# Optimization experiments

Measured on AMD Instinct MI355X. Metric: run time of the kernel, lower is better.

Reference implementation:

```python
import jax, jax.numpy as jnp
import numpy as np

TEMPERATURE = 0.07
NEG = -1e9  # stand-in for -inf on the diagonal; exp(NEG) == 0


def setup_inputs() -> dict:
    key = jax.random.key(0)
    k1, k2, k3 = jax.random.split(key, 3)
    B, D = 4096, 1024
    return {
        "anchor_features": jax.random.normal(k1, (B, D), dtype=jnp.float32),
        "positive_features": jax.random.normal(k2, (B, D), dtype=jnp.float32),
        "labels": jax.random.randint(k3, (B,), 0, 2),
    }


def reference(anchor_features, positive_features, labels):
    B = anchor_features.shape[0]
    # L2-normalize (normalize=True)
    a = anchor_features / jnp.linalg.norm(anchor_features, axis=1, keepdims=True)
    p = positive_features / jnp.linalg.norm(positive_features, axis=1, keepdims=True)
    feats = jnp.concatenate([a, p], axis=0)                      # [2B, D]
    sim = jnp.matmul(feats, feats.T) / TEMPERATURE               # [2B, 2B]
    diag = jnp.eye(2 * B, dtype=bool)
    sim = jnp.where(diag, NEG, sim)                              # mask self-similarity
    # logsumexp over all non-self entries per row (diag contributes exp(NEG)=0)
    lse = jax.nn.logsumexp(sim, axis=1)                          # [2B]
    # positive pair similarity: sim[i, i+B] == sim[i+B, i] == <a_i, p_i>/t
    cross = jnp.sum(a * p, axis=1) / TEMPERATURE                 # [B]
    pos_sim = jnp.concatenate([cross, cross])                    # [2B]
    lab = jnp.concatenate([labels, labels]).astype(sim.dtype)    # [2B], 0/1
    per_row = (-pos_sim + lse) * lab
    num_pos = jnp.sum(lab)
    return jnp.where(num_pos > 0, jnp.sum(per_row) / num_pos, jnp.float32(0.0))
```

## Files before the change

kernel.cpp:

```cpp
#include <hip/hip_runtime.h>
#include <hip/hip_bf16.h>

#define TEMP_INV (1.0f / 0.07f)
#define LOG2E 1.4426950408889634f
#define LN2 0.6931471805599453f
#define CFIX 21.0f

typedef __attribute__((ext_vector_type(4))) float f32x4;

__device__ __forceinline__ void gload16(const unsigned char* g,
                                        unsigned char* l) {
  __builtin_amdgcn_global_load_lds(
      (const __attribute__((address_space(1))) void*)g,
      (__attribute__((address_space(3))) void*)l, 16, 0, 0);
}

__global__ __launch_bounds__(256) void norm_kernel(
    const float* __restrict__ A, const float* __restrict__ P,
    unsigned char* __restrict__ F, float* __restrict__ cross,
    float* __restrict__ lsum, int B, int D) {
  const int row = blockIdx.x;
  const int t = threadIdx.x;
  {
    const int zi = row * 256 + t;
    if (zi < 2 * B) lsum[zi] = 0.f;
  }
  const float4* a4 = reinterpret_cast<const float4*>(A + (size_t)row * D);
  const float4* p4 = reinterpret_cast<const float4*>(P + (size_t)row * D);
  const int n4 = D >> 2;
  float sa = 0.f, sp = 0.f, sx = 0.f;
  for (int i = t; i < n4; i += 256) {
    float4 av = a4[i], pv = p4[i];
    sa += av.x * av.x + av.y * av.y + av.z * av.z + av.w * av.w;
    sp += pv.x * pv.x + pv.y * pv.y + pv.z * pv.z + pv.w * pv.w;
    sx += av.x * pv.x + av.y * pv.y + av.z * pv.z + av.w * pv.w;
  }
#pragma unroll
  for (int off = 32; off; off >>= 1) {
    sa += __shfl_down(sa, off);
    sp += __shfl_down(sp, off);
    sx += __shfl_down(sx, off);
  }
  __shared__ float red[3][4];
  const int wid = t >> 6, lane = t & 63;
  if (lane == 0) { red[0][wid] = sa; red[1][wid] = sp; red[2][wid] = sx; }
  __syncthreads();
  sa = red[0][0] + red[0][1] + red[0][2] + red[0][3];
  sp = red[1][0] + red[1][1] + red[1][2] + red[1][3];
  sx = red[2][0] + red[2][1] + red[2][2] + red[2][3];
  const float ian = rsqrtf(sa), ipn = rsqrtf(sp);
  const float ia = ian * 16.f, ip = ipn * 16.f;
  unsigned char* fa = F + (size_t)row * D;
  unsigned char* fp = F + (size_t)(B + row) * D;
  for (int i = t; i < n4; i += 256) {
    float4 av = a4[i], pv = p4[i];
    int qa = 0, qp = 0;
    qa = __builtin_amdgcn_cvt_pk_fp8_f32(av.x * ia, av.y * ia, qa, false);
    qa = __builtin_amdgcn_cvt_pk_fp8_f32(av.z * ia, av.w * ia, qa, true);
    qp = __builtin_amdgcn_cvt_pk_fp8_f32(pv.x * ip, pv.y * ip, qp, false);
    qp = __builtin_amdgcn_cvt_pk_fp8_f32(pv.z * ip, pv.w * ip, qp, true);
    reinterpret_cast<int*>(fa)[i] = qa;
    reinterpret_cast<int*>(fp)[i] = qp;
  }
  if (t == 0) cross[row] = sx * ian * ipn;
}


__device__ __forceinline__ void gram_tile(
    unsigned char* LDS8, const unsigned char* F, float* lsum, int D,
    int r0, int c0, bool diag) {
  const int t = threadIdx.x;
  const int lane = t & 63, w = t >> 6;
  const int lo = lane & 15, hi = lane >> 4;
  const int wr = w >> 2, wn = w & 3;

  const int KSa = t >> 9;
  const int cS = t & 511;
  const int lineS = cS >> 3, pS = (cS & 7) ^ (lineS & 7);
  const int trS = lineS * 4 + (pS >> 1);
  const int kcS = ((pS & 1) << 4) + KSa * 32;
  const unsigned char* sA = F + (size_t)(c0 + trS) * D + kcS;
  const unsigned char* sB = F + (size_t)(r0 + trS) * D + kcS;
  const int dstW = (w & 7) * 1024;

  int offA[4], offB[4];
#pragma unroll
  for (int mf = 0; mf < 4; ++mf) {
    const int r = wr * 64 + mf * 16 + lo;
    const int lr = r >> 2;
    const int cu = ((r & 3) << 1) | (hi >> 1);
    offA[mf] = lr * 128 + ((cu ^ (lr & 7)) << 4) + ((hi & 1) << 3);
  }
#pragma unroll
  for (int nf = 0; nf < 4; ++nf) {
    const int r = wn * 64 + nf * 16 + lo;
    const int lr = r >> 2;
    const int cu = ((r & 3) << 1) | (hi >> 1);
    offB[nf] = lr * 128 + ((cu ^ (lr & 7)) << 4) + ((hi & 1) << 3);
  }

#define STAGE(V)                                                        \
  do {                                                                  \
    int v_ = (V); if (v_ > 15) v_ = 15;                                 \
    gload16(sA + v_ * 64,                                               \
            LDS8 + ((V) & 3) * 32768 + KSa * 8192 + dstW);              \
    gload16(sB + v_ * 64,                                               \
            LDS8 + ((V) & 3) * 32768 + 16384 + KSa * 8192 + dstW);      \
  } while (0)

  f32x4 acc[4][4];
#pragma unroll
  for (int a = 0; a < 4; ++a)
#pragma unroll
    for (int bb = 0; bb < 4; ++bb) acc[a][bb] = (f32x4){0.f, 0.f, 0.f, 0.f};

  STAGE(0); STAGE(1); STAGE(2);

  for (int v = 0; v < 16; ++v) {
    const int buf = v & 3;
    asm volatile("s_waitcnt vmcnt(4)" ::: "memory");
    __builtin_amdgcn_s_barrier();
    asm volatile("" ::: "memory");

    long a0[4], a1[4], b0[4], b1[4];
#pragma unroll
    for (int q = 0; q < 4; ++q) {
      b0[q] = *(const long*)(LDS8 + buf * 32768 + 16384 + offB[q]);
      a0[q] = *(const long*)(LDS8 + buf * 32768 + offA[q]);
      b1[q] = *(const long*)(LDS8 + buf * 32768 + 16384 + 8192 + offB[q]);
      a1[q] = *(const long*)(LDS8 + buf * 32768 + 8192 + offA[q]);
    }

    STAGE(v + 3);

    __builtin_amdgcn_s_setprio(1);
#pragma unroll
    for (int mf = 0; mf < 4; ++mf)
#pragma unroll
      for (int nf = 0; nf < 4; ++nf)
        acc[mf][nf] = __builtin_amdgcn_mfma_f32_16x16x32_fp8_fp8(
            a0[mf], b0[nf], acc[mf][nf], 0, 0, 0);
#pragma unroll
    for (int mf = 0; mf < 4; ++mf)
#pragma unroll
      for (int nf = 0; nf < 4; ++nf)
        acc[mf][nf] = __builtin_amdgcn_mfma_f32_16x16x32_fp8_fp8(
            a1[mf], b1[nf], acc[mf][nf], 0, 0, 0);
    __builtin_amdgcn_s_setprio(0);
    asm volatile("" ::: "memory");
  }

  const float scl = LOG2E * TEMP_INV / 256.f;
  float s_i[4] = {0.f, 0.f, 0.f, 0.f};
  float s_j[16];
#pragma unroll
  for (int q = 0; q < 16; ++q) s_j[q] = 0.f;
  {
    const int dgb = (r0 + wn * 64) - (c0 + wr * 64);
#pragma unroll
    for (int nf = 0; nf < 4; ++nf) {
      const int dg = dgb + nf * 16 + lo;
#pragma unroll
      for (int mf = 0; mf < 4; ++mf)
#pragma unroll
        for (int rg = 0; rg < 4; ++rg) {
          const int jloc = mf * 16 + hi * 4 + rg;
          float e = exp2f(acc[mf][nf][rg] * scl - CFIX);
          if (diag && dg == jloc) e = 0.f;
          s_i[nf] += e;
          s_j[mf * 4 + rg] += e;
        }
    }
  }
#pragma unroll
  for (int nf = 0; nf < 4; ++nf) {
    float v = s_i[nf];
    v += __shfl_xor(v, 16);
    v += __shfl_xor(v, 32);
    if (hi == 0) atomicAdd(&lsum[r0 + wn * 64 + nf * 16 + lo], v);
  }
  if (!diag) {
#pragma unroll
    for (int q = 0; q < 16; ++q) {
      float v = s_j[q];
      v += __shfl_xor(v, 1);
      v += __shfl_xor(v, 2);
      v += __shfl_xor(v, 4);
      v += __shfl_xor(v, 8);
      if (lo == 0)
        atomicAdd(&lsum[c0 + wr * 64 + (q >> 2) * 16 + hi * 4 + (q & 3)], v);
    }
  }
  asm volatile("s_waitcnt vmcnt(0)" ::: "memory");
  __builtin_amdgcn_s_barrier();
  asm volatile("" ::: "memory");
#undef STAGE
}

__global__ __launch_bounds__(1024) void gram_full_kernel(
    const unsigned char* __restrict__ F, float* __restrict__ lsum, int NN,
    int D) {
  __shared__ unsigned char lds8[4][2][2][8192];
  const int bid = blockIdx.x;
  const int nT = (bid < 16) ? 2 : 1;

  for (int ti = 0; ti < nT; ++ti) {
    int lin;
    if (ti == 0) {
      lin = bid;
      lin = (lin & 7) * 64 + (lin >> 3);
    } else {
      lin = 512 + bid;
    }
    int by = (int)((sqrtf(8.f * (float)lin + 1.f) - 1.f) * 0.5f);
    while ((by + 1) * (by + 2) / 2 <= lin) ++by;
    while (by * (by + 1) / 2 > lin) --by;
    const int bx = lin - by * (by + 1) / 2;
    const int r0 = bx * 256;
    const int c0 = by * 256;
    const bool diag = (bx == by);
    gram_tile(&lds8[0][0][0][0], F, lsum, D, r0, c0, diag);
  }
}

__global__ __launch_bounds__(256) void finalize_part(
    const float* __restrict__ lsum, const float* __restrict__ cross,
    const int* __restrict__ labels, float* __restrict__ bsum,
    float* __restrict__ bcnt, int B) {
  const int NN = 2 * B;
  const int i = blockIdx.x * 256 + threadIdx.x;
  float sum = 0.f, cnt = 0.f;
  if (i < NN) {
    const float lse = LN2 * (CFIX + log2f(lsum[i]));
    const float lab = (float)labels[i % B];
    sum = (lse - cross[i % B] * TEMP_INV) * lab;
    cnt = lab;
  }
#pragma unroll
  for (int off = 32; off; off >>= 1) {
    sum += __shfl_down(sum, off);
    cnt += __shfl_down(cnt, off);
  }
  __shared__ float rs[4], rc[4];
  const int wid = threadIdx.x >> 6, lane = threadIdx.x & 63;
  if (lane == 0) { rs[wid] = sum; rc[wid] = cnt; }
  __syncthreads();
  if (threadIdx.x == 0) {
    bsum[blockIdx.x] = rs[0] + rs[1] + rs[2] + rs[3];
    bcnt[blockIdx.x] = rc[0] + rc[1] + rc[2] + rc[3];
  }
}

__global__ __launch_bounds__(64) void finalize_final(
    const float* __restrict__ bsum, const float* __restrict__ bcnt,
    float* __restrict__ out, int nb) {
  const int t = threadIdx.x;
  float s = (t < nb) ? bsum[t] : 0.f;
  float c = (t < nb) ? bcnt[t] : 0.f;
#pragma unroll
  for (int off = 32; off; off >>= 1) {
    s += __shfl_down(s, off);
    c += __shfl_down(c, off);
  }
  if (t == 0) out[0] = (c > 0.f) ? s / c : 0.f;
}

extern "C" void kernel_launch(void* const* d_in, const int* in_sizes, int n_in,
                              void* d_out, int out_size, void* d_ws, size_t ws_size,
                              hipStream_t stream) {
  const float* A = (const float*)d_in[0];
  const float* P = (const float*)d_in[1];
  const int* labels = (const int*)d_in[2];
  float* out = (float*)d_out;
  const int B = in_sizes[2];
  const int D = in_sizes[0] / B;
  const int NN = 2 * B;

  char* ws = (char*)d_ws;
  unsigned char* F = (unsigned char*)ws;
  size_t off = (size_t)NN * D;
  off = (off + 255) & ~(size_t)255;
  float* cross = (float*)(ws + off);
  off += (size_t)B * sizeof(float);
  off = (off + 255) & ~(size_t)255;
  float* lsum = (float*)(ws + off);
  off += (size_t)NN * sizeof(float);
  off = (off + 255) & ~(size_t)255;
  float* bsum = (float*)(ws + off);
  off += 64 * sizeof(float);
  float* bcnt = (float*)(ws + off);

  norm_kernel<<<B, 256, 0, stream>>>(A, P, F, cross, lsum, B, D);
  gram_full_kernel<<<512, 1024, 0, stream>>>(F, lsum, NN, D);
  const int nb = (NN + 255) / 256;
  finalize_part<<<nb, 256, 0, stream>>>(lsum, cross, labels, bsum, bcnt, B);
  finalize_final<<<1, 64, 0, stream>>>(bsum, bcnt, out, nb);
}
```

Measured before the change: 115.7 us.

## Pre-swizzle fp8 features into MFMA fragment layout and drop LDS staging

The norm kernel now writes the quantized features in a blocked layout that matches the MFMA operand fragments, so each lane can load its 8-byte operand directly from global memory. The gram kernel drops the LDS async-copy pipeline and barriers in favour of register double-buffering. It also moves from 256x256 tiles with 1024 threads to 128x128 tiles with 256 threads and many more blocks. This removes LDS traffic and synchronisation, but every wave now reads its operands from L2/global with less reuse per block and more total global traffic.

New measurement: 145.5 us. 25.8% more time.

```diff
diff --git a/kernel.cpp b/kernel.cpp
--- a/kernel.cpp
+++ b/kernel.cpp
@@ -8,16 +8,9 @@
 
 typedef __attribute__((ext_vector_type(4))) float f32x4;
 
-__device__ __forceinline__ void gload16(const unsigned char* g,
-                                        unsigned char* l) {
-  __builtin_amdgcn_global_load_lds(
-      (const __attribute__((address_space(1))) void*)g,
-      (__attribute__((address_space(3))) void*)l, 16, 0, 0);
-}
-
 __global__ __launch_bounds__(256) void norm_kernel(
     const float* __restrict__ A, const float* __restrict__ P,
-    unsigned char* __restrict__ F, float* __restrict__ cross,
+    unsigned char* __restrict__ Fr, float* __restrict__ cross,
     float* __restrict__ lsum, int B, int D) {
   const int row = blockIdx.x;
   const int t = threadIdx.x;
@@ -50,8 +43,12 @@
   sx = red[2][0] + red[2][1] + red[2][2] + red[2][3];
   const float ian = rsqrtf(sa), ipn = rsqrtf(sp);
   const float ia = ian * 16.f, ip = ipn * 16.f;
-  unsigned char* fa = F + (size_t)row * D;
-  unsigned char* fp = F + (size_t)(B + row) * D;
+  const int NN16 = (2 * B) >> 4;
+  const size_t KBSTR = (size_t)NN16 * 512;
+  const int kb = t >> 3, hi = (t >> 1) & 3, half = (t & 1) * 4;
+  const int rbA = row >> 4, rbP = (B + row) >> 4;
+  const int lo = row & 15;
+  const size_t off8 = (size_t)kb * KBSTR + ((hi << 4) + lo) * 8 + half;
   for (int i = t; i < n4; i += 256) {
     float4 av = a4[i], pv = p4[i];
     int qa = 0, qp = 0;
@@ -59,54 +56,37 @@
     qa = __builtin_amdgcn_cvt_pk_fp8_f32(av.z * ia, av.w * ia, qa, true);
     qp = __builtin_amdgcn_cvt_pk_fp8_f32(pv.x * ip, pv.y * ip, qp, false);
     qp = __builtin_amdgcn_cvt_pk_fp8_f32(pv.z * ip, pv.w * ip, qp, true);
-    reinterpret_cast<int*>(fa)[i] = qa;
-    reinterpret_cast<int*>(fp)[i] = qp;
+    *reinterpret_cast<int*>(Fr + off8 + (size_t)rbA * 512) = qa;
+    *reinterpret_cast<int*>(Fr + off8 + (size_t)rbP * 512) = qp;
   }
   if (t == 0) cross[row] = sx * ian * ipn;
 }
 
-
-__device__ __forceinline__ void gram_tile(
-    unsigned char* LDS8, const unsigned char* F, float* lsum, int D,
-    int r0, int c0, bool diag) {
+__global__ __launch_bounds__(256, 4) void gram_kernel(
+    const unsigned char* __restrict__ Fr, float* __restrict__ lsum, int NN,
+    int D) {
+  const int nrb = NN >> 7;
+  const int ntri = nrb * (nrb + 1) / 2;
+  int lin = blockIdx.x;
+  lin = (lin & 7) * (ntri >> 3) + (lin >> 3);
+  int by = (int)((sqrtf(8.f * (float)lin + 1.f) - 1.f) * 0.5f);
+  while ((by + 1) * (by + 2) / 2 <= lin) ++by;
+  while (by * (by + 1) / 2 > lin) --by;
+  const int bx = lin - by * (by + 1) / 2;
+  const int r0 = bx * 128;
+  const int c0 = by * 128;
+  const bool diag = (bx == by);
+
   const int t = threadIdx.x;
   const int lane = t & 63, w = t >> 6;
   const int lo = lane & 15, hi = lane >> 4;
-  const int wr = w >> 2, wn = w & 3;
-
-  const int KSa = t >> 9;
-  const int cS = t & 511;
-  const int lineS = cS >> 3, pS = (cS & 7) ^ (lineS & 7);
-  const int trS = lineS * 4 + (pS >> 1);
-  const int kcS = ((pS & 1) << 4) + KSa * 32;
-  const unsigned char* sA = F + (size_t)(c0 + trS) * D + kcS;
-  const unsigned char* sB = F + (size_t)(r0 + trS) * D + kcS;
-  const int dstW = (w & 7) * 1024;
-
-  int offA[4], offB[4];
-#pragma unroll
-  for (int mf = 0; mf < 4; ++mf) {
-    const int r = wr * 64 + mf * 16 + lo;
-    const int lr = r >> 2;
-    const int cu = ((r & 3) << 1) | (hi >> 1);
-    offA[mf] = lr * 128 + ((cu ^ (lr & 7)) << 4) + ((hi & 1) << 3);
-  }
-#pragma unroll
-  for (int nf = 0; nf < 4; ++nf) {
-    const int r = wn * 64 + nf * 16 + lo;
-    const int lr = r >> 2;
-    const int cu = ((r & 3) << 1) | (hi >> 1);
-    offB[nf] = lr * 128 + ((cu ^ (lr & 7)) << 4) + ((hi & 1) << 3);
-  }
-
-#define STAGE(V)                                                        \
-  do {                                                                  \
-    int v_ = (V); if (v_ > 15) v_ = 15;                                 \
-    gload16(sA + v_ * 64,                                               \
-            LDS8 + ((V) & 3) * 32768 + KSa * 8192 + dstW);              \
-    gload16(sB + v_ * 64,                                               \
-            LDS8 + ((V) & 3) * 32768 + 16384 + KSa * 8192 + dstW);      \
-  } while (0)
+  const int wr = w >> 1, wn = w & 1;
+
+  const size_t KBSTR = (size_t)(NN >> 4) * 512;
+  const unsigned char* pA =
+      Fr + (size_t)((c0 >> 4) + wr * 4) * 512 + (size_t)lane * 8;
+  const unsigned char* pB =
+      Fr + (size_t)((r0 >> 4) + wn * 4) * 512 + (size_t)lane * 8;
 
   f32x4 acc[4][4];
 #pragma unroll
@@ -114,40 +94,44 @@
 #pragma unroll
     for (int bb = 0; bb < 4; ++bb) acc[a][bb] = (f32x4){0.f, 0.f, 0.f, 0.f};
 
-  STAGE(0); STAGE(1); STAGE(2);
-
-  for (int v = 0; v < 16; ++v) {
-    const int buf = v & 3;
-    asm volatile("s_waitcnt vmcnt(4)" ::: "memory");
-    __builtin_amdgcn_s_barrier();
-    asm volatile("" ::: "memory");
-
-    long a0[4], a1[4], b0[4], b1[4];
+  long aP[4], bP[4], aQ[4], bQ[4];
+#pragma unroll
+  for (int q = 0; q < 4; ++q) {
+    aP[q] = *(const long*)(pA + q * 512);
+    bP[q] = *(const long*)(pB + q * 512);
+  }
+
+  for (int kb = 0; kb < 32; kb += 2) {
 #pragma unroll
     for (int q = 0; q < 4; ++q) {
-      b0[q] = *(const long*)(LDS8 + buf * 32768 + 16384 + offB[q]);
-      a0[q] = *(const long*)(LDS8 + buf * 32768 + offA[q]);
-      b1[q] = *(const long*)(LDS8 + buf * 32768 + 16384 + 8192 + offB[q]);
-      a1[q] = *(const long*)(LDS8 + buf * 32768 + 8192 + offA[q]);
-    }
-
-    STAGE(v + 3);
-
+      aQ[q] = *(const long*)(pA + KBSTR + q * 512);
+      bQ[q] = *(const long*)(pB + KBSTR + q * 512);
+    }
     __builtin_amdgcn_s_setprio(1);
 #pragma unroll
     for (int mf = 0; mf < 4; ++mf)
 #pragma unroll
       for (int nf = 0; nf < 4; ++nf)
         acc[mf][nf] = __builtin_amdgcn_mfma_f32_16x16x32_fp8_fp8(
-            a0[mf], b0[nf], acc[mf][nf], 0, 0, 0);
+            aP[mf], bP[nf], acc[mf][nf], 0, 0, 0);
+    __builtin_amdgcn_s_setprio(0);
+    pA += 2 * KBSTR;
+    pB += 2 * KBSTR;
+    if (kb + 2 < 32) {
+#pragma unroll
+      for (int q = 0; q < 4; ++q) {
+        aP[q] = *(const long*)(pA + q * 512);
+        bP[q] = *(const long*)(pB + q * 512);
+      }
+    }
+    __builtin_amdgcn_s_setprio(1);
 #pragma unroll
     for (int mf = 0; mf < 4; ++mf)
 #pragma unroll
       for (int nf = 0; nf < 4; ++nf)
         acc[mf][nf] = __builtin_amdgcn_mfma_f32_16x16x32_fp8_fp8(
-            a1[mf], b1[nf], acc[mf][nf], 0, 0, 0);
+            aQ[mf], bQ[nf], acc[mf][nf], 0, 0, 0);
     __builtin_amdgcn_s_setprio(0);
-    asm volatile("" ::: "memory");
   }
 
   const float scl = LOG2E * TEMP_INV / 256.f;
@@ -190,36 +174,6 @@
       if (lo == 0)
         atomicAdd(&lsum[c0 + wr * 64 + (q >> 2) * 16 + hi * 4 + (q & 3)], v);
     }
-  }
-  asm volatile("s_waitcnt vmcnt(0)" ::: "memory");
-  __builtin_amdgcn_s_barrier();
-  asm volatile("" ::: "memory");
-#undef STAGE
-}
-
-__global__ __launch_bounds__(1024) void gram_full_kernel(
-    const unsigned char* __restrict__ F, float* __restrict__ lsum, int NN,
-    int D) {
-  __shared__ unsigned char lds8[4][2][2][8192];
-  const int bid = blockIdx.x;
-  const int nT = (bid < 16) ? 2 : 1;
-
-  for (int ti = 0; ti < nT; ++ti) {
-    int lin;
-    if (ti == 0) {
-      lin = bid;
-      lin = (lin & 7) * 64 + (lin >> 3);
-    } else {
-      lin = 512 + bid;
-    }
-    int by = (int)((sqrtf(8.f * (float)lin + 1.f) - 1.f) * 0.5f);
-    while ((by + 1) * (by + 2) / 2 <= lin) ++by;
-    while (by * (by + 1) / 2 > lin) --by;
-    const int bx = lin - by * (by + 1) / 2;
-    const int r0 = bx * 256;
-    const int c0 = by * 256;
-    const bool diag = (bx == by);
-    gram_tile(&lds8[0][0][0][0], F, lsum, D, r0, c0, diag);
   }
 }
 
@@ -277,7 +231,7 @@
   const int NN = 2 * B;
 
   char* ws = (char*)d_ws;
-  unsigned char* F = (unsigned char*)ws;
+  unsigned char* Fr = (unsigned char*)ws;
   size_t off = (size_t)NN * D;
   off = (off + 255) & ~(size_t)255;
   float* cross = (float*)(ws + off);
@@ -290,8 +244,10 @@
   off += 64 * sizeof(float);
   float* bcnt = (float*)(ws + off);
 
-  norm_kernel<<<B, 256, 0, stream>>>(A, P, F, cross, lsum, B, D);
-  gram_full_kernel<<<512, 1024, 0, stream>>>(F, lsum, NN, D);
+  norm_kernel<<<B, 256, 0, stream>>>(A, P, Fr, cross, lsum, B, D);
+  const int nrb = NN >> 7;
+  const int ntri = nrb * (nrb + 1) / 2;
+  gram_kernel<<<ntri, 256, 0, stream>>>(Fr, lsum, NN, D);
   const int nb = (NN + 255) / 256;
   finalize_part<<<nb, 256, 0, stream>>>(lsum, cross, labels, bsum, bcnt, B);
   finalize_final<<<1, 64, 0, stream>>>(bsum, bcnt, out, nb);
```
